# Kernel tuning notes

Measured on AMD Instinct MI355X. Metric: run time of the kernel, lower is better.

Reference implementation:

```python
import jax, jax.numpy as jnp
import numpy as np
import math

NUM_HEADS = 8
CANTOR_DEPTH = 8
LOCAL_WINDOW = 16


def _cantor_routes(T, depth=CANTOR_DEPTH, window=LOCAL_WINDOW):
    # Vectorized Cantor coordinate per position, then top-k nearest neighbors.
    pos = jnp.arange(T, dtype=jnp.float32)
    x = jnp.clip(pos / max(1, T - 1), 1e-6, 1.0 - 1e-6)
    c = jnp.zeros_like(x)
    factor = 0.5
    for _ in range(depth):
        x = x * 3.0
        digit = jnp.floor(x)
        x = x - digit
        c = c + factor * (digit == 2.0).astype(jnp.float32)
        factor *= 0.5
    dist = jnp.abs(c[:, None] - c[None, :])  # [T, T]
    _, idx = jax.lax.top_k(-dist, min(window, T))  # smallest distances
    return idx  # [T, window] int32


def setup_inputs() -> dict:
    key = jax.random.key(0)
    ks = jax.random.split(key, 10)
    B, T, D = 2, 4096, 512
    s = 1.0 / math.sqrt(D)
    return {
        "x": jax.random.normal(ks[0], (B, T, D), dtype=jnp.float32),
        "Wq": jax.random.normal(ks[1], (D, D), dtype=jnp.float32) * s,
        "bq": jnp.zeros((D,), dtype=jnp.float32),
        "Wk": jax.random.normal(ks[2], (D, D), dtype=jnp.float32) * s,
        "bk": jnp.zeros((D,), dtype=jnp.float32),
        "Wv": jax.random.normal(ks[3], (D, D), dtype=jnp.float32) * s,
        "bv": jnp.zeros((D,), dtype=jnp.float32),
        "Wo": jax.random.normal(ks[4], (D, D), dtype=jnp.float32) * s,
        "bo": jnp.zeros((D,), dtype=jnp.float32),
        "temperature": jnp.float32(0.07),
    }


def reference(x, Wq, bq, Wk, bk, Wv, bv, Wo, bo, temperature):
    B, T, D = x.shape
    H = NUM_HEADS
    hd = D // H

    def proj(W, b):
        return (x @ W + b).reshape(B, T, H, hd).transpose(0, 2, 1, 3)  # [B,H,T,hd]

    Q = proj(Wq, bq)
    K = proj(Wk, bk)
    V = proj(Wv, bv)

    routes = _cantor_routes(T)  # [T, W]
    k_n = K[:, :, routes, :]  # [B,H,T,W,hd] gather of routed neighbors
    v_n = V[:, :, routes, :]

    scale = math.sqrt(hd) * jnp.abs(temperature)
    scores = jnp.einsum('bhtd,bhtwd->bhtw', Q, k_n) / scale
    attn = jax.nn.softmax(scores, axis=-1)
    out = jnp.einsum('bhtw,bhtwd->bhtd', attn, v_n)  # [B,H,T,hd]
    out = out.transpose(0, 2, 1, 3).reshape(B, T, D)
    return out @ Wo + bo
```

## Files before the change

### kernel.cpp

```cpp
#include <hip/hip_runtime.h>
#include <hip/hip_bf16.h>
#include <cstdint>
#include <climits>

#define TT 4096
#define DD 512
#define HH 8
#define HD 64
#define WW 16
#define CDEPTH 8

typedef unsigned short ushortT;
typedef unsigned int uintT;
using bf16x8 = __attribute__((ext_vector_type(8))) short;
using f32x4  = __attribute__((ext_vector_type(4))) float;

static __device__ __forceinline__ uintT f2bf(float v) {
    __hip_bfloat16 h = __float2bfloat16(v);
    return (uintT)*reinterpret_cast<ushortT*>(&h);
}
static __device__ __forceinline__ float bf2f(uintT u) {
    return __uint_as_float(u << 16);
}

static __device__ __forceinline__ int swz_idx(int r, int c) {
    const int u = r >> 1;
    const int s = (((r & 1) << 2) | c) ^ (u & 7);
    return (u << 6) + (s << 3);
}
static __device__ __forceinline__ void inv_swz(int p, int& r, int& c) {
    const int u = p >> 3;
    const int bits = (p & 7) ^ (u & 7);
    r = (u << 1) | (bits >> 2);
    c = bits & 3;
}

#define GLDS(gsrc, ldst)                                                          \
    __builtin_amdgcn_global_load_lds(                                             \
        (const __attribute__((address_space(1))) uint32_t*)(gsrc),                \
        (__attribute__((address_space(3))) uint32_t*)(ldst), 16, 0, 0)

static __device__ __forceinline__ int cantor_m(int t) {
    float x = (float)t / (float)(TT - 1);
    x = fminf(fmaxf(x, 1e-6f), 1.0f - 1e-6f);
    int m = 0;
    #pragma unroll
    for (int i = 0; i < CDEPTH; ++i) {
        float x3 = x * 3.0f;
        float dg = floorf(x3);
        x = x3 - dg;
        m = (m << 1) | ((dg == 2.0f) ? 1 : 0);
    }
    return m;
}

__global__ __launch_bounds__(256) void routes_f16_kernel(int* __restrict__ kv_g,
                                                         int* __restrict__ cnt_g,
                                                         int* __restrict__ f16_g) {
    __shared__ int kvloc[TT];
    __shared__ int pscan[256];
    const int tid = threadIdx.x;
    const int b = blockIdx.x;

    #pragma unroll
    for (int i = 0; i < 16; ++i) {
        const int t = i * 256 + tid;
        kvloc[t] = cantor_m(t);
    }
    __syncthreads();

    if (tid < 16) kv_g[b * 16 + tid] = kvloc[b * 16 + tid];

    int localcnt = 0;
    #pragma unroll
    for (int i = 0; i < 16; ++i)
        localcnt += (kvloc[tid * 16 + i] == b) ? 1 : 0;

    pscan[tid] = localcnt;
    __syncthreads();
    #pragma unroll
    for (int off = 1; off < 256; off <<= 1) {
        int v = (tid >= off) ? pscan[tid - off] : 0;
        __syncthreads();
        pscan[tid] += v;
        __syncthreads();
    }
    const int excl = pscan[tid] - localcnt;

    int r = excl;
    #pragma unroll
    for (int i = 0; i < 16; ++i) {
        const int t = tid * 16 + i;
        if (kvloc[t] == b) {
            if (r < 16) f16_g[b * 16 + r] = t;
            ++r;
        }
    }
    if (tid == 255) cnt_g[b] = pscan[255];
}

__global__ __launch_bounds__(256) void routes_merge_kernel(const int* __restrict__ cnt_g,
                                                           const int* __restrict__ f16_g,
                                                           int* __restrict__ table) {
    __shared__ int cnt[256];
    __shared__ int f16[256][16];
    const int tid = threadIdx.x;
    cnt[tid] = cnt_g[tid];
    {
        int4 a = reinterpret_cast<const int4*>(f16_g)[tid * 4 + 0];
        int4 b4 = reinterpret_cast<const int4*>(f16_g)[tid * 4 + 1];
        int4 c4 = reinterpret_cast<const int4*>(f16_g)[tid * 4 + 2];
        int4 d4 = reinterpret_cast<const int4*>(f16_g)[tid * 4 + 3];
        f16[tid][0] = a.x;  f16[tid][1] = a.y;  f16[tid][2] = a.z;  f16[tid][3] = a.w;
        f16[tid][4] = b4.x; f16[tid][5] = b4.y; f16[tid][6] = b4.z; f16[tid][7] = b4.w;
        f16[tid][8] = c4.x; f16[tid][9] = c4.y; f16[tid][10] = c4.z; f16[tid][11] = c4.w;
        f16[tid][12] = d4.x; f16[tid][13] = d4.y; f16[tid][14] = d4.z; f16[tid][15] = d4.w;
    }
    __syncthreads();

    int rtl[WW];
    int n = 0;
    {
        int c = cnt[tid];
        int take = (c < WW) ? c : WW;
        for (int i = 0; i < take; ++i) rtl[n++] = f16[tid][i];
    }
    for (int d = 1; n < WW && d <= 256; ++d) {
        const int lo = tid - d, hi = tid + d;
        const int clo = (lo >= 0) ? cnt[lo] : 0;
        const int chi = (hi < 256) ? cnt[hi] : 0;
        const int need = WW - n;
        if (clo + chi <= need) {
            for (int i = 0; i < clo; ++i) rtl[n++] = f16[lo][i];
            for (int i = 0; i < chi; ++i) rtl[n++] = f16[hi][i];
        } else {
            const int cl = (clo < WW) ? clo : WW;
            const int ch = (chi < WW) ? chi : WW;
            int i = 0, j = 0;
            while (n < WW) {
                int a = (i < cl) ? f16[lo][i] : INT_MAX;
                int b = (j < ch) ? f16[hi][j] : INT_MAX;
                if (a < b) { rtl[n++] = a; ++i; }
                else       { rtl[n++] = b; ++j; }
            }
        }
    }
    #pragma unroll
    for (int i = 0; i < WW; ++i) table[tid * WW + i] = rtl[i];
}

__global__ __launch_bounds__(256) void convw_tile_kernel(
        const float* __restrict__ W0, const float* __restrict__ W1,
        const float* __restrict__ W2, const float* __restrict__ W3,
        ushortT* __restrict__ H0, ushortT* __restrict__ L0,
        ushortT* __restrict__ H1, ushortT* __restrict__ L1,
        ushortT* __restrict__ H2, ushortT* __restrict__ L2,
        ushortT* __restrict__ H3, ushortT* __restrict__ L3) {
    const float* src; ushortT* dh; ushortT* dl;
    switch (blockIdx.z) {
        case 0: src = W0; dh = H0; dl = L0; break;
        case 1: src = W1; dh = H1; dl = L1; break;
        case 2: src = W2; dh = H2; dl = L2; break;
        default: src = W3; dh = H3; dl = L3; break;
    }
    const int nt = blockIdx.x;
    const int kt = blockIdx.y;
    const size_t tilebase = ((size_t)(nt * 16 + kt)) * 4096;

    #pragma unroll
    for (int s = 0; s < 2; ++s) {
        const int p = threadIdx.x + s * 256;
        int r, c;
        inv_swz(p, r, c);
        const int n = nt * 128 + r;
        const int k = kt * 32 + c * 8;
        uintT rh[8], rl[8];
        #pragma unroll
        for (int j = 0; j < 8; ++j) {
            const float f = src[(size_t)(k + j) * DD + n];
            const uintT h = f2bf(f);
            rh[j] = h;
            rl[j] = f2bf(f - bf2f(h));
        }
        uint4 oh, ol;
        oh.x = rh[0] | (rh[1] << 16); oh.y = rh[2] | (rh[3] << 16);
        oh.z = rh[4] | (rh[5] << 16); oh.w = rh[6] | (rh[7] << 16);
        ol.x = rl[0] | (rl[1] << 16); ol.y = rl[2] | (rl[3] << 16);
        ol.z = rl[4] | (rl[5] << 16); ol.w = rl[6] | (rl[7] << 16);
        *reinterpret_cast<uint4*>(&dh[tilebase + (size_t)p * 8]) = oh;
        *reinterpret_cast<uint4*>(&dl[tilebase + (size_t)p * 8]) = ol;
    }
}

#define QBM 64
#define QBN 128
#define QBK 32
#define QKV_NWG 1536
#define OUT_NWG 512

__global__ __launch_bounds__(256, 6) void qkv_gemm(const float* __restrict__ x,
        const ushortT* __restrict__ Wqh, const ushortT* __restrict__ Wql,
        const ushortT* __restrict__ Wkh, const ushortT* __restrict__ Wkl,
        const ushortT* __restrict__ Wvh, const ushortT* __restrict__ Wvl,
        const float* __restrict__ bq, const float* __restrict__ bk, const float* __restrict__ bv,
        float* __restrict__ Qo, float* __restrict__ Ko, ushortT* __restrict__ Vo, int M) {
    __shared__ short Ash[QBM * QBK];
    __shared__ short Asl[QBM * QBK];
    __shared__ short Bsh[QBN * QBK];
    __shared__ short Bsl[QBN * QBK];
    const int tid = threadIdx.x;
    const int lane = tid & 63;
    const int wid = tid >> 6;

    const int id = blockIdx.x;
    const int swz = (id & 7) * (QKV_NWG / 8) + (id >> 3);
    const int bm = (swz / 12) * QBM;
    const int bnG = (swz % 12) * QBN;
    const int seg = bnG >> 9;
    const int bn = bnG & 511;
    const ushortT* __restrict__ Bhp = (seg == 0) ? Wqh : (seg == 1) ? Wkh : Wvh;
    const ushortT* __restrict__ Blp = (seg == 0) ? Wql : (seg == 1) ? Wkl : Wvl;
    const float* __restrict__ bias = (seg == 0) ? bq : (seg == 1) ? bk : bv;

    const int wr = wid >> 1;
    const int wc = wid & 1;

    f32x4 acc[2][4];
    #pragma unroll
    for (int i = 0; i < 2; ++i)
        #pragma unroll
        for (int j = 0; j < 4; ++j)
            acc[i][j] = (f32x4){0.f, 0.f, 0.f, 0.f};

    const int arow = tid >> 2;
    const int achk = tid & 3;
    const int fr = lane & 15;
    const int kq = lane >> 4;
    const int nt = bn >> 7;

    for (int k0 = 0; k0 < DD; k0 += QBK) {
        {
            const size_t tb = ((size_t)(nt * 16 + (k0 >> 5))) * 4096;
            const int base = wid * 128;
            #pragma unroll
            for (int q = 0; q < 2; ++q) {
                const size_t so = tb + (size_t)(base + q * 64 + lane) * 8;
                GLDS(&Bhp[so], &Bsh[(base + q * 64) * 8]);
                GLDS(&Blp[so], &Bsl[(base + q * 64) * 8]);
            }
        }
        {
            const float* srcp = &x[(size_t)(bm + arow) * DD + k0 + achk * 8];
            const float4 v0 = *reinterpret_cast<const float4*>(srcp);
            const float4 v1 = *reinterpret_cast<const float4*>(srcp + 4);
            const float vv[8] = {v0.x, v0.y, v0.z, v0.w, v1.x, v1.y, v1.z, v1.w};
            bf16x8 vh, vl;
            #pragma unroll
            for (int j = 0; j < 8; ++j) {
                uintT h = f2bf(vv[j]);
                vh[j] = (short)h;
                vl[j] = (short)f2bf(vv[j] - bf2f(h));
            }
            const int ai = swz_idx(arow, achk);
            *reinterpret_cast<bf16x8*>(&Ash[ai]) = vh;
            *reinterpret_cast<bf16x8*>(&Asl[ai]) = vl;
        }
        __syncthreads();
        {
            bf16x8 avh[2], avl[2], bvh[4], bvl[4];
            #pragma unroll
            for (int i = 0; i < 2; ++i) {
                const int ai = swz_idx(wr * 32 + i * 16 + fr, kq);
                avh[i] = *reinterpret_cast<const bf16x8*>(&Ash[ai]);
                avl[i] = *reinterpret_cast<const bf16x8*>(&Asl[ai]);
            }
            #pragma unroll
            for (int j = 0; j < 4; ++j) {
                const int bi = swz_idx(wc * 64 + j * 16 + fr, kq);
                bvh[j] = *reinterpret_cast<const bf16x8*>(&Bsh[bi]);
                bvl[j] = *reinterpret_cast<const bf16x8*>(&Bsl[bi]);
            }
            #pragma unroll
            for (int i = 0; i < 2; ++i)
                #pragma unroll
                for (int j = 0; j < 4; ++j) {
                    acc[i][j] = __builtin_amdgcn_mfma_f32_16x16x32_bf16(avh[i], bvh[j], acc[i][j], 0, 0, 0);
                    acc[i][j] = __builtin_amdgcn_mfma_f32_16x16x32_bf16(avl[i], bvh[j], acc[i][j], 0, 0, 0);
                    acc[i][j] = __builtin_amdgcn_mfma_f32_16x16x32_bf16(avh[i], bvl[j], acc[i][j], 0, 0, 0);
                }
        }
        __syncthreads();
    }

    const int fq = lane >> 4;
    #pragma unroll
    for (int j = 0; j < 4; ++j) {
        const int col = bn + wc * 64 + j * 16 + fr;
        const float bvv = bias[col];
        #pragma unroll
        for (int i = 0; i < 2; ++i) {
            const int row0 = bm + wr * 32 + i * 16 + fq * 4;
            #pragma unroll
            for (int r = 0; r < 4; ++r) {
                const float val = acc[i][j][r] + bvv;
                if (seg == 2) {
                    Vo[(size_t)(row0 + r) * DD + col] = (ushortT)f2bf(val);
                } else {
                    float* dst = seg ? Ko : Qo;
                    dst[(size_t)(row0 + r) * DD + col] = val;
                }
            }
        }
    }
}

__global__ __launch_bounds__(256, 6) void out_gemm(const ushortT* __restrict__ Ahg,
                                                   const ushortT* __restrict__ Alg,
                                                   const ushortT* __restrict__ Bh,
                                                   const ushortT* __restrict__ Bl,
                                                   const float* __restrict__ bias,
                                                   float* __restrict__ C, int M) {
    __shared__ short Ash[QBM * QBK];
    __shared__ short Asl[QBM * QBK];
    __shared__ short Bsh[QBN * QBK];
    __shared__ short Bsl[QBN * QBK];
    const int tid = threadIdx.x;
    const int lane = tid & 63;
    const int wid = tid >> 6;

    const int id = blockIdx.x;
    const int swz = (id & 7) * (OUT_NWG / 8) + (id >> 3);
    const int bm = (swz >> 2) * QBM;
    const int bn = (swz & 3) * QBN;
    const int wr = wid >> 1;
    const int wc = wid & 1;

    f32x4 acc[2][4];
    #pragma unroll
    for (int i = 0; i < 2; ++i)
        #pragma unroll
        for (int j = 0; j < 4; ++j)
            acc[i][j] = (f32x4){0.f, 0.f, 0.f, 0.f};

    const int arow = tid >> 2;
    const int achk = tid & 3;
    const int fr = lane & 15;
    const int kq = lane >> 4;
    const int nt = bn >> 7;

    for (int k0 = 0; k0 < DD; k0 += QBK) {
        {
            const size_t tb = ((size_t)(nt * 16 + (k0 >> 5))) * 4096;
            const int base = wid * 128;
            #pragma unroll
            for (int q = 0; q < 2; ++q) {
                const size_t so = tb + (size_t)(base + q * 64 + lane) * 8;
                GLDS(&Bh[so], &Bsh[(base + q * 64) * 8]);
                GLDS(&Bl[so], &Bsl[(base + q * 64) * 8]);
            }
        }
        {
            const size_t g = (size_t)(bm + arow) * DD + k0 + achk * 8;
            const int ai = swz_idx(arow, achk);
            *reinterpret_cast<bf16x8*>(&Ash[ai]) = *reinterpret_cast<const bf16x8*>(&Ahg[g]);
            *reinterpret_cast<bf16x8*>(&Asl[ai]) = *reinterpret_cast<const bf16x8*>(&Alg[g]);
        }
        __syncthreads();
        {
            bf16x8 avh[2], avl[2], bvh[4], bvl[4];
            #pragma unroll
            for (int i = 0; i < 2; ++i) {
                const int ai = swz_idx(wr * 32 + i * 16 + fr, kq);
                avh[i] = *reinterpret_cast<const bf16x8*>(&Ash[ai]);
                avl[i] = *reinterpret_cast<const bf16x8*>(&Asl[ai]);
            }
            #pragma unroll
            for (int j = 0; j < 4; ++j) {
                const int bi = swz_idx(wc * 64 + j * 16 + fr, kq);
                bvh[j] = *reinterpret_cast<const bf16x8*>(&Bsh[bi]);
                bvl[j] = *reinterpret_cast<const bf16x8*>(&Bsl[bi]);
            }
            #pragma unroll
            for (int i = 0; i < 2; ++i)
                #pragma unroll
                for (int j = 0; j < 4; ++j) {
                    acc[i][j] = __builtin_amdgcn_mfma_f32_16x16x32_bf16(avh[i], bvh[j], acc[i][j], 0, 0, 0);
                    acc[i][j] = __builtin_amdgcn_mfma_f32_16x16x32_bf16(avl[i], bvh[j], acc[i][j], 0, 0, 0);
                    acc[i][j] = __builtin_amdgcn_mfma_f32_16x16x32_bf16(avh[i], bvl[j], acc[i][j], 0, 0, 0);
                }
        }
        __syncthreads();
    }

    const int fq = lane >> 4;
    #pragma unroll
    for (int j = 0; j < 4; ++j) {
        const int col = bn + wc * 64 + j * 16 + fr;
        const float bvv = bias[col];
        #pragma unroll
        for (int i = 0; i < 2; ++i) {
            const int row0 = bm + wr * 32 + i * 16 + fq * 4;
            #pragma unroll
            for (int r = 0; r < 4; ++r)
                C[(size_t)(row0 + r) * DD + col] = acc[i][j][r] + bvv;
        }
    }
}

__global__ __launch_bounds__(256) void attn2_kernel(const float* __restrict__ Q,
                                                    const float* __restrict__ K,
                                                    const ushortT* __restrict__ V,
                                                    const int* __restrict__ kv_g,
                                                    const int* __restrict__ table,
                                                    const float* __restrict__ temp_ptr,
                                                    ushortT* __restrict__ AOh,
                                                    ushortT* __restrict__ AOl, int B) {
    const int lane = threadIdx.x & 63;
    const int u = (blockIdx.x * blockDim.x + threadIdx.x) >> 6;
    if (u >= B * TT) return;
    const int t = u & (TT - 1);
    const float scale_inv = 1.0f / (8.0f * fabsf(temp_ptr[0]));

    const int* rt = &table[kv_g[t] * WW];
    int sidx[WW];
    #pragma unroll
    for (int w = 0; w < WW; ++w) sidx[w] = rt[w];

    const size_t rowbase = (size_t)u * DD + lane * 8;
    const size_t bbase = (size_t)(u - t) * DD;
    const float4 q0 = *reinterpret_cast<const float4*>(&Q[rowbase]);
    const float4 q1 = *reinterpret_cast<const float4*>(&Q[rowbase + 4]);

    float sc[WW];
    #pragma unroll
    for (int w = 0; w < WW; ++w) {
        const float* kr = &K[bbase + (size_t)sidx[w] * DD + lane * 8];
        const float4 k0 = *reinterpret_cast<const float4*>(kr);
        const float4 k1 = *reinterpret_cast<const float4*>(kr + 4);
        float p = q0.x * k0.x + q0.y * k0.y + q0.z * k0.z + q0.w * k0.w
                + q1.x * k1.x + q1.y * k1.y + q1.z * k1.z + q1.w * k1.w;
        p += __shfl_xor(p, 1);
        p += __shfl_xor(p, 2);
        p += __shfl_xor(p, 4);
        sc[w] = p * scale_inv;
    }

    float m = sc[0];
    #pragma unroll
    for (int w = 1; w < WW; ++w) m = fmaxf(m, sc[w]);
    float pr[WW];
    float sum = 0.0f;
    #pragma unroll
    for (int w = 0; w < WW; ++w) { pr[w] = expf(sc[w] - m); sum += pr[w]; }
    const float inv = 1.0f / sum;

    float o[8] = {0.f, 0.f, 0.f, 0.f, 0.f, 0.f, 0.f, 0.f};
    #pragma unroll
    for (int w = 0; w < WW; ++w) {
        const uint4 vv = *reinterpret_cast<const uint4*>(&V[bbase + (size_t)sidx[w] * DD + lane * 8]);
        o[0] += pr[w] * bf2f(vv.x & 0xffffu); o[1] += pr[w] * bf2f(vv.x >> 16);
        o[2] += pr[w] * bf2f(vv.y & 0xffffu); o[3] += pr[w] * bf2f(vv.y >> 16);
        o[4] += pr[w] * bf2f(vv.z & 0xffffu); o[5] += pr[w] * bf2f(vv.z >> 16);
        o[6] += pr[w] * bf2f(vv.w & 0xffffu); o[7] += pr[w] * bf2f(vv.w >> 16);
    }
    uintT rh[8], rl[8];
    #pragma unroll
    for (int i = 0; i < 8; ++i) {
        const float val = o[i] * inv;
        uintT h = f2bf(val);
        rh[i] = h;
        rl[i] = f2bf(val - bf2f(h));
    }
    uint4 oh, ol;
    oh.x = rh[0] | (rh[1] << 16); oh.y = rh[2] | (rh[3] << 16);
    oh.z = rh[4] | (rh[5] << 16); oh.w = rh[6] | (rh[7] << 16);
    ol.x = rl[0] | (rl[1] << 16); ol.y = rl[2] | (rl[3] << 16);
    ol.z = rl[4] | (rl[5] << 16); ol.w = rl[6] | (rl[7] << 16);
    *reinterpret_cast<uint4*>(&AOh[rowbase]) = oh;
    *reinterpret_cast<uint4*>(&AOl[rowbase]) = ol;
}

extern "C" void kernel_launch(void* const* d_in, const int* in_sizes, int n_in,
                              void* d_out, int out_size, void* d_ws, size_t ws_size,
                              hipStream_t stream) {
    const float* x    = (const float*)d_in[0];
    const float* Wq   = (const float*)d_in[1];
    const float* bq   = (const float*)d_in[2];
    const float* Wk   = (const float*)d_in[3];
    const float* bk   = (const float*)d_in[4];
    const float* Wv   = (const float*)d_in[5];
    const float* bv   = (const float*)d_in[6];
    const float* Wo   = (const float*)d_in[7];
    const float* bo   = (const float*)d_in[8];
    const float* temp = (const float*)d_in[9];
    float* out = (float*)d_out;

    const int B = in_sizes[0] / (TT * DD);
    const int M = B * TT;
    const size_t MD = (size_t)M * DD;

    float* Qb = (float*)d_ws;
    float* Kb = Qb + MD;
    ushortT* Vb = (ushortT*)(Kb + MD);
    ushortT* AOh = Vb + MD;
    ushortT* AOl = AOh + MD;
    ushortT* Wqh = AOl + MD;
    ushortT* Wql = Wqh + DD * DD;
    ushortT* Wkh = Wql + DD * DD;
    ushortT* Wkl = Wkh + DD * DD;
    ushortT* Wvh = Wkl + DD * DD;
    ushortT* Wvl = Wvh + DD * DD;
    ushortT* Woh = Wvl + DD * DD;
    ushortT* Wol = Woh + DD * DD;
    int* kvg   = (int*)(Wol + DD * DD);
    int* table = kvg + TT;
    int* cntg  = table + 256 * WW;
    int* f16g  = cntg + 256;

    routes_f16_kernel<<<256, 256, 0, stream>>>(kvg, cntg, f16g);
    routes_merge_kernel<<<1, 256, 0, stream>>>(cntg, f16g, table);
    convw_tile_kernel<<<dim3(4, 16, 4), 256, 0, stream>>>(Wq, Wk, Wv, Wo,
                                                          Wqh, Wql, Wkh, Wkl,
                                                          Wvh, Wvl, Woh, Wol);

    qkv_gemm<<<QKV_NWG, 256, 0, stream>>>(x, Wqh, Wql, Wkh, Wkl, Wvh, Wvl,
                                          bq, bk, bv, Qb, Kb, Vb, M);

    attn2_kernel<<<(M * 64) / 256, 256, 0, stream>>>(Qb, Kb, Vb, kvg, table, temp, AOh, AOl, B);

    out_gemm<<<OUT_NWG, 256, 0, stream>>>(AOh, AOl, Woh, Wol, bo, out, M);
}
```

Before: 142.6 us.

## Double-buffer LDS tiles in QKV GEMM to overlap loads with MFMA

The QKV projection GEMM now keeps two LDS stages and issues the global loads and fp32-to-bf16 hi/lo split for the next K tile before running the MFMAs on the current one. This replaces two barriers per K step with one. The goal is to hide global memory latency behind compute. The cost is twice the LDS footprint and launch bounds lowered from 6 to 3 blocks per CU, which reduces occupancy.

```diff
diff --git a/kernel.cpp b/kernel.cpp
--- a/kernel.cpp
+++ b/kernel.cpp
@@ -195,19 +195,75 @@
 #define QBM 64
 #define QBN 128
 #define QBK 32
+#define ASZ (QBM * QBK)
+#define BSZ (QBN * QBK)
 #define QKV_NWG 1536
 #define OUT_NWG 512
 
-__global__ __launch_bounds__(256, 6) void qkv_gemm(const float* __restrict__ x,
+#define STAGE_QKV(bufIdx, kt_)                                                    \
+    {                                                                             \
+        const int boff = (bufIdx) * BSZ;                                          \
+        const size_t tb = ((size_t)(nt * 16 + (kt_))) * 4096;                     \
+        const int base = wid * 128;                                               \
+        _Pragma("unroll")                                                         \
+        for (int q = 0; q < 2; ++q) {                                             \
+            const size_t so = tb + (size_t)(base + q * 64 + lane) * 8;            \
+            GLDS(&Bhp[so], &Bsh[boff + (base + q * 64) * 8]);                     \
+            GLDS(&Blp[so], &Bsl[boff + (base + q * 64) * 8]);                     \
+        }                                                                         \
+        const float* srcp = &x[(size_t)(bm + arow) * DD + (kt_) * 32 + achk * 8]; \
+        const float4 v0 = *reinterpret_cast<const float4*>(srcp);                 \
+        const float4 v1 = *reinterpret_cast<const float4*>(srcp + 4);             \
+        const float vv[8] = {v0.x, v0.y, v0.z, v0.w, v1.x, v1.y, v1.z, v1.w};     \
+        bf16x8 vh, vl;                                                            \
+        _Pragma("unroll")                                                         \
+        for (int j = 0; j < 8; ++j) {                                             \
+            uintT h = f2bf(vv[j]);                                                \
+            vh[j] = (short)h;                                                     \
+            vl[j] = (short)f2bf(vv[j] - bf2f(h));                                 \
+        }                                                                         \
+        const int ai = (bufIdx) * ASZ + swz_idx(arow, achk);                      \
+        *reinterpret_cast<bf16x8*>(&Ash[ai]) = vh;                                \
+        *reinterpret_cast<bf16x8*>(&Asl[ai]) = vl;                                \
+    }
+
+#define COMPUTE_QKV(bufIdx)                                                       \
+    {                                                                             \
+        const int aoff = (bufIdx) * ASZ;                                          \
+        const int boff = (bufIdx) * BSZ;                                          \
+        bf16x8 avh[2], avl[2], bvh[4], bvl[4];                                    \
+        _Pragma("unroll")                                                         \
+        for (int i = 0; i < 2; ++i) {                                             \
+            const int ai = aoff + swz_idx(wr * 32 + i * 16 + fr, kq);             \
+            avh[i] = *reinterpret_cast<const bf16x8*>(&Ash[ai]);                  \
+            avl[i] = *reinterpret_cast<const bf16x8*>(&Asl[ai]);                  \
+        }                                                                         \
+        _Pragma("unroll")                                                         \
+        for (int j = 0; j < 4; ++j) {                                             \
+            const int bi = boff + swz_idx(wc * 64 + j * 16 + fr, kq);             \
+            bvh[j] = *reinterpret_cast<const bf16x8*>(&Bsh[bi]);                  \
+            bvl[j] = *reinterpret_cast<const bf16x8*>(&Bsl[bi]);                  \
+        }                                                                         \
+        _Pragma("unroll")                                                         \
+        for (int i = 0; i < 2; ++i)                                               \
+            _Pragma("unroll")                                                     \
+            for (int j = 0; j < 4; ++j) {                                         \
+                acc[i][j] = __builtin_amdgcn_mfma_f32_16x16x32_bf16(avh[i], bvh[j], acc[i][j], 0, 0, 0); \
+                acc[i][j] = __builtin_amdgcn_mfma_f32_16x16x32_bf16(avl[i], bvh[j], acc[i][j], 0, 0, 0); \
+                acc[i][j] = __builtin_amdgcn_mfma_f32_16x16x32_bf16(avh[i], bvl[j], acc[i][j], 0, 0, 0); \
+            }                                                                     \
+    }
+
+__global__ __launch_bounds__(256, 3) void qkv_gemm(const float* __restrict__ x,
         const ushortT* __restrict__ Wqh, const ushortT* __restrict__ Wql,
         const ushortT* __restrict__ Wkh, const ushortT* __restrict__ Wkl,
         const ushortT* __restrict__ Wvh, const ushortT* __restrict__ Wvl,
         const float* __restrict__ bq, const float* __restrict__ bk, const float* __restrict__ bv,
         float* __restrict__ Qo, float* __restrict__ Ko, ushortT* __restrict__ Vo, int M) {
-    __shared__ short Ash[QBM * QBK];
-    __shared__ short Asl[QBM * QBK];
-    __shared__ short Bsh[QBN * QBK];
-    __shared__ short Bsl[QBN * QBK];
+    __shared__ short Ash[2 * ASZ];
+    __shared__ short Asl[2 * ASZ];
+    __shared__ short Bsh[2 * BSZ];
+    __shared__ short Bsl[2 * BSZ];
     const int tid = threadIdx.x;
     const int lane = tid & 63;
     const int wid = tid >> 6;
@@ -238,6 +294,75 @@
     const int kq = lane >> 4;
     const int nt = bn >> 7;
 
+    STAGE_QKV(0, 0)
+    __syncthreads();
+
+    int cur = 0;
+    #pragma unroll 1
+    for (int t = 0; t < 15; ++t) {
+        STAGE_QKV(cur ^ 1, t + 1)
+        COMPUTE_QKV(cur)
+        __syncthreads();
+        cur ^= 1;
+    }
+    COMPUTE_QKV(cur)
+
+    const int fq = lane >> 4;
+    #pragma unroll
+    for (int j = 0; j < 4; ++j) {
+        const int col = bn + wc * 64 + j * 16 + fr;
+        const float bvv = bias[col];
+        #pragma unroll
+        for (int i = 0; i < 2; ++i) {
+            const int row0 = bm + wr * 32 + i * 16 + fq * 4;
+            #pragma unroll
+            for (int r = 0; r < 4; ++r) {
+                const float val = acc[i][j][r] + bvv;
+                if (seg == 2) {
+                    Vo[(size_t)(row0 + r) * DD + col] = (ushortT)f2bf(val);
+                } else {
+                    float* dst = seg ? Ko : Qo;
+                    dst[(size_t)(row0 + r) * DD + col] = val;
+                }
+            }
+        }
+    }
+}
+
+__global__ __launch_bounds__(256, 6) void out_gemm(const ushortT* __restrict__ Ahg,
+                                                   const ushortT* __restrict__ Alg,
+                                                   const ushortT* __restrict__ Bh,
+                                                   const ushortT* __restrict__ Bl,
+                                                   const float* __restrict__ bias,
+                                                   float* __restrict__ C, int M) {
+    __shared__ short Ash[QBM * QBK];
+    __shared__ short Asl[QBM * QBK];
+    __shared__ short Bsh[QBN * QBK];
+    __shared__ short Bsl[QBN * QBK];
+    const int tid = threadIdx.x;
+    const int lane = tid & 63;
+    const int wid = tid >> 6;
+
+    const int id = blockIdx.x;
+    const int swz = (id & 7) * (OUT_NWG / 8) + (id >> 3);
+    const int bm = (swz >> 2) * QBM;
+    const int bn = (swz & 3) * QBN;
+    const int wr = wid >> 1;
+    const int wc = wid & 1;
+
+    f32x4 acc[2][4];
+    #pragma unroll
+    for (int i = 0; i < 2; ++i)
+        #pragma unroll
+        for (int j = 0; j < 4; ++j)
+            acc[i][j] = (f32x4){0.f, 0.f, 0.f, 0.f};
+
+    const int arow = tid >> 2;
+    const int achk = tid & 3;
+    const int fr = lane & 15;
+    const int kq = lane >> 4;
+    const int nt = bn >> 7;
+
     for (int k0 = 0; k0 < DD; k0 += QBK) {
         {
             const size_t tb = ((size_t)(nt * 16 + (k0 >> 5))) * 4096;
@@ -245,25 +370,15 @@
             #pragma unroll
             for (int q = 0; q < 2; ++q) {
                 const size_t so = tb + (size_t)(base + q * 64 + lane) * 8;
-                GLDS(&Bhp[so], &Bsh[(base + q * 64) * 8]);
-                GLDS(&Blp[so], &Bsl[(base + q * 64) * 8]);
+                GLDS(&Bh[so], &Bsh[(base + q * 64) * 8]);
+                GLDS(&Bl[so], &Bsl[(base + q * 64) * 8]);
             }
         }
         {
-            const float* srcp = &x[(size_t)(bm + arow) * DD + k0 + achk * 8];
-            const float4 v0 = *reinterpret_cast<const float4*>(srcp);
-            const float4 v1 = *reinterpret_cast<const float4*>(srcp + 4);
-            const float vv[8] = {v0.x, v0.y, v0.z, v0.w, v1.x, v1.y, v1.z, v1.w};
-            bf16x8 vh, vl;
-            #pragma unroll
-            for (int j = 0; j < 8; ++j) {
-                uintT h = f2bf(vv[j]);
-                vh[j] = (short)h;
-                vl[j] = (short)f2bf(vv[j] - bf2f(h));
-            }
+            const size_t g = (size_t)(bm + arow) * DD + k0 + achk * 8;
             const int ai = swz_idx(arow, achk);
-            *reinterpret_cast<bf16x8*>(&Ash[ai]) = vh;
-            *reinterpret_cast<bf16x8*>(&Asl[ai]) = vl;
+            *reinterpret_cast<bf16x8*>(&Ash[ai]) = *reinterpret_cast<const bf16x8*>(&Ahg[g]);
+            *reinterpret_cast<bf16x8*>(&Asl[ai]) = *reinterpret_cast<const bf16x8*>(&Alg[g]);
         }
         __syncthreads();
         {
@@ -301,106 +416,6 @@
         for (int i = 0; i < 2; ++i) {
             const int row0 = bm + wr * 32 + i * 16 + fq * 4;
             #pragma unroll
-            for (int r = 0; r < 4; ++r) {
-                const float val = acc[i][j][r] + bvv;
-                if (seg == 2) {
-                    Vo[(size_t)(row0 + r) * DD + col] = (ushortT)f2bf(val);
-                } else {
-                    float* dst = seg ? Ko : Qo;
-                    dst[(size_t)(row0 + r) * DD + col] = val;
-                }
-            }
-        }
-    }
-}
-
-__global__ __launch_bounds__(256, 6) void out_gemm(const ushortT* __restrict__ Ahg,
-                                                   const ushortT* __restrict__ Alg,
-                                                   const ushortT* __restrict__ Bh,
-                                                   const ushortT* __restrict__ Bl,
-                                                   const float* __restrict__ bias,
-                                                   float* __restrict__ C, int M) {
-    __shared__ short Ash[QBM * QBK];
-    __shared__ short Asl[QBM * QBK];
-    __shared__ short Bsh[QBN * QBK];
-    __shared__ short Bsl[QBN * QBK];
-    const int tid = threadIdx.x;
-    const int lane = tid & 63;
-    const int wid = tid >> 6;
-
-    const int id = blockIdx.x;
-    const int swz = (id & 7) * (OUT_NWG / 8) + (id >> 3);
-    const int bm = (swz >> 2) * QBM;
-    const int bn = (swz & 3) * QBN;
-    const int wr = wid >> 1;
-    const int wc = wid & 1;
-
-    f32x4 acc[2][4];
-    #pragma unroll
-    for (int i = 0; i < 2; ++i)
-        #pragma unroll
-        for (int j = 0; j < 4; ++j)
-            acc[i][j] = (f32x4){0.f, 0.f, 0.f, 0.f};
-
-    const int arow = tid >> 2;
-    const int achk = tid & 3;
-    const int fr = lane & 15;
-    const int kq = lane >> 4;
-    const int nt = bn >> 7;
-
-    for (int k0 = 0; k0 < DD; k0 += QBK) {
-        {
-            const size_t tb = ((size_t)(nt * 16 + (k0 >> 5))) * 4096;
-            const int base = wid * 128;
-            #pragma unroll
-            for (int q = 0; q < 2; ++q) {
-                const size_t so = tb + (size_t)(base + q * 64 + lane) * 8;
-                GLDS(&Bh[so], &Bsh[(base + q * 64) * 8]);
-                GLDS(&Bl[so], &Bsl[(base + q * 64) * 8]);
-            }
-        }
-        {
-            const size_t g = (size_t)(bm + arow) * DD + k0 + achk * 8;
-            const int ai = swz_idx(arow, achk);
-            *reinterpret_cast<bf16x8*>(&Ash[ai]) = *reinterpret_cast<const bf16x8*>(&Ahg[g]);
-            *reinterpret_cast<bf16x8*>(&Asl[ai]) = *reinterpret_cast<const bf16x8*>(&Alg[g]);
-        }
-        __syncthreads();
-        {
-            bf16x8 avh[2], avl[2], bvh[4], bvl[4];
-            #pragma unroll
-            for (int i = 0; i < 2; ++i) {
-                const int ai = swz_idx(wr * 32 + i * 16 + fr, kq);
-                avh[i] = *reinterpret_cast<const bf16x8*>(&Ash[ai]);
-                avl[i] = *reinterpret_cast<const bf16x8*>(&Asl[ai]);
-            }
-            #pragma unroll
-            for (int j = 0; j < 4; ++j) {
-                const int bi = swz_idx(wc * 64 + j * 16 + fr, kq);
-                bvh[j] = *reinterpret_cast<const bf16x8*>(&Bsh[bi]);
-                bvl[j] = *reinterpret_cast<const bf16x8*>(&Bsl[bi]);
-            }
-            #pragma unroll
-            for (int i = 0; i < 2; ++i)
-                #pragma unroll
-                for (int j = 0; j < 4; ++j) {
-                    acc[i][j] = __builtin_amdgcn_mfma_f32_16x16x32_bf16(avh[i], bvh[j], acc[i][j], 0, 0, 0);
-                    acc[i][j] = __builtin_amdgcn_mfma_f32_16x16x32_bf16(avl[i], bvh[j], acc[i][j], 0, 0, 0);
-                    acc[i][j] = __builtin_amdgcn_mfma_f32_16x16x32_bf16(avh[i], bvl[j], acc[i][j], 0, 0, 0);
-                }
-        }
-        __syncthreads();
-    }
-
-    const int fq = lane >> 4;
-    #pragma unroll
-    for (int j = 0; j < 4; ++j) {
-        const int col = bn + wc * 64 + j * 16 + fr;
-        const float bvv = bias[col];
-        #pragma unroll
-        for (int i = 0; i < 2; ++i) {
-            const int row0 = bm + wr * 32 + i * 16 + fq * 4;
-            #pragma unroll
             for (int r = 0; r < 4; ++r)
                 C[(size_t)(row0 + r) * DD + col] = acc[i][j][r] + bvv;
         }
```

Result: slower. 147.5 us (+3.5%).
